# Kernel tuning notes

Hardware: AMD Instinct MI355X
Metric: run time of the kernel (lower is better)

## Reference

```python
import jax, jax.numpy as jnp
import numpy as np

EXTENT = (7, 7)
STRIDE = 1.0
H_IMG, W_IMG, C_IMG = 256, 256, 256
N_BOXES = 1000


def setup_inputs() -> dict:
    key = jax.random.key(0)
    k_img, k_a, k_b = jax.random.split(key, 3)
    image = jax.random.normal(k_img, (1, H_IMG, W_IMG, C_IMG), dtype=jnp.float32)
    # metadata row: (h, w, scale)
    metadata = jnp.array([[float(H_IMG), float(W_IMG), 1.0]], dtype=jnp.float32)
    # valid boxes in pixel coords (x1, y1, x2, y2) with x1<x2, y1<y2
    pa = jax.random.uniform(k_a, (1, N_BOXES, 4), dtype=jnp.float32) * (W_IMG - 1)
    pb = jax.random.uniform(k_b, (1, N_BOXES, 4), dtype=jnp.float32) * (W_IMG - 1)
    lo = jnp.minimum(pa, pb)
    hi = jnp.maximum(pa, pb) + 1.0
    boxes = jnp.stack([lo[..., 0], lo[..., 1],
                       jnp.clip(hi[..., 0], 0, W_IMG - 1),
                       jnp.clip(hi[..., 1], 0, H_IMG - 1)], axis=-1)
    return {"metadata": metadata, "image": image, "boxes": boxes}


def _crop_and_resize(img, nboxes, gh, gw):
    # img: [H, W, C]; nboxes: [N, 4] normalized (y1, x1, y2, x2)
    H, W, C = img.shape
    y1, x1, y2, x2 = nboxes[:, 0], nboxes[:, 1], nboxes[:, 2], nboxes[:, 3]
    ty = jnp.arange(gh, dtype=img.dtype) / (gh - 1)  # [gh]
    tx = jnp.arange(gw, dtype=img.dtype) / (gw - 1)  # [gw]
    in_y = (y1[:, None] + ty[None, :] * (y2 - y1)[:, None]) * (H - 1)  # [N, gh]
    in_x = (x1[:, None] + tx[None, :] * (x2 - x1)[:, None]) * (W - 1)  # [N, gw]
    valid_y = (in_y >= 0) & (in_y <= H - 1)
    valid_x = (in_x >= 0) & (in_x <= W - 1)
    y0f = jnp.floor(in_y)
    x0f = jnp.floor(in_x)
    ly = (in_y - y0f)[:, :, None, None]   # [N, gh, 1, 1]
    lx = (in_x - x0f)[:, None, :, None]   # [N, 1, gw, 1]
    y0 = jnp.clip(y0f, 0, H - 1).astype(jnp.int32)
    y1i = jnp.clip(y0f + 1, 0, H - 1).astype(jnp.int32)
    x0 = jnp.clip(x0f, 0, W - 1).astype(jnp.int32)
    x1i = jnp.clip(x0f + 1, 0, W - 1).astype(jnp.int32)
    yy0, yy1 = y0[:, :, None], y1i[:, :, None]  # [N, gh, 1]
    xx0, xx1 = x0[:, None, :], x1i[:, None, :]  # [N, 1, gw]
    g00 = img[yy0, xx0]  # [N, gh, gw, C]
    g01 = img[yy0, xx1]
    g10 = img[yy1, xx0]
    g11 = img[yy1, xx1]
    top = g00 * (1 - lx) + g01 * lx
    bot = g10 * (1 - lx) + g11 * lx
    out = top * (1 - ly) + bot * ly
    mask = (valid_y[:, :, None] & valid_x[:, None, :])[..., None]
    return jnp.where(mask, out, jnp.zeros((), dtype=img.dtype))


def reference(metadata, image, boxes):
    gh, gw = EXTENT
    b = boxes.astype(jnp.float32) / STRIDE
    h = metadata[0, 0]
    w = metadata[0, 1]
    x1 = b[..., 0] / (w - 1)
    y1 = b[..., 1] / (h - 1)
    x2 = b[..., 2] / (w - 1)
    y2 = b[..., 3] / (h - 1)
    nboxes = jnp.stack([y1, x1, y2, x2], axis=-1).reshape(-1, 4)  # [N, 4]
    slices = _crop_and_resize(image[0], nboxes, gh, gw)  # [N, gh, gw, C]
    return slices[None]  # [1, N, gh, gw, C]
```

## Files before the change

kernel.cpp:

```cpp
#include <hip/hip_runtime.h>

#define GH 7
#define GW 7
#define HIMG 256
#define WIMG 256
#define CIMG 256
#define NBOXES 1000
#define NCELLS (NBOXES * GH * GW)

typedef float f32x4 __attribute__((ext_vector_type(4)));

__global__ __launch_bounds__(256) void roi_kernel(
    const float* __restrict__ meta,
    const float* __restrict__ img,
    const float* __restrict__ boxes,
    float* __restrict__ out)
{
    const int wave = threadIdx.x >> 6;
    const int lane = threadIdx.x & 63;
    const int cell = blockIdx.x * 4 + wave;

    const int b  = cell / (GH * GW);
    const int g  = cell - b * (GH * GW);
    const int gy = g / GW;
    const int gx = g - gy * GW;

    const float h = meta[0];
    const float w = meta[1];

    const float bx1 = boxes[b * 4 + 0] / (w - 1.0f);
    const float by1 = boxes[b * 4 + 1] / (h - 1.0f);
    const float bx2 = boxes[b * 4 + 2] / (w - 1.0f);
    const float by2 = boxes[b * 4 + 3] / (h - 1.0f);

    const float ty = (float)gy / (float)(GH - 1);
    const float tx = (float)gx / (float)(GW - 1);

    const float in_y = (by1 + ty * (by2 - by1)) * (float)(HIMG - 1);
    const float in_x = (bx1 + tx * (bx2 - bx1)) * (float)(WIMG - 1);

    const bool valid = (in_y >= 0.0f) && (in_y <= (float)(HIMG - 1)) &&
                       (in_x >= 0.0f) && (in_x <= (float)(WIMG - 1));

    const float y0f = floorf(in_y);
    const float x0f = floorf(in_x);
    const float ly = in_y - y0f;
    const float lx = in_x - x0f;

    const int y0 = (int)fminf(fmaxf(y0f,        0.0f), (float)(HIMG - 1));
    const int y1 = (int)fminf(fmaxf(y0f + 1.0f, 0.0f), (float)(HIMG - 1));
    const int x0 = (int)fminf(fmaxf(x0f,        0.0f), (float)(WIMG - 1));
    const int x1 = (int)fminf(fmaxf(x0f + 1.0f, 0.0f), (float)(WIMG - 1));

    const f32x4* p00 = (const f32x4*)(img + (size_t)(y0 * WIMG + x0) * CIMG) + lane;
    const f32x4* p01 = (const f32x4*)(img + (size_t)(y0 * WIMG + x1) * CIMG) + lane;
    const f32x4* p10 = (const f32x4*)(img + (size_t)(y1 * WIMG + x0) * CIMG) + lane;
    const f32x4* p11 = (const f32x4*)(img + (size_t)(y1 * WIMG + x1) * CIMG) + lane;

    const f32x4 g00 = *p00;
    const f32x4 g01 = *p01;
    const f32x4 g10 = *p10;
    const f32x4 g11 = *p11;

    const float omlx = 1.0f - lx;
    const float omly = 1.0f - ly;

    f32x4 o = (g00 * omlx + g01 * lx) * omly + (g10 * omlx + g11 * lx) * ly;

    if (!valid) {
        o = (f32x4)0.0f;
    }

    f32x4* op = (f32x4*)(out + (size_t)cell * CIMG) + lane;
    __builtin_nontemporal_store(o, op);
}

extern "C" void kernel_launch(void* const* d_in, const int* in_sizes, int n_in,
                              void* d_out, int out_size, void* d_ws, size_t ws_size,
                              hipStream_t stream) {
    const float* meta  = (const float*)d_in[0];
    const float* img   = (const float*)d_in[1];
    const float* boxes = (const float*)d_in[2];
    float* out = (float*)d_out;

    dim3 grid(NCELLS / 4);
    dim3 block(256);
    roi_kernel<<<grid, block, 0, stream>>>(meta, img, boxes, out);
}
```

Measured before the change: 123.8 us.

## Process two cells per wave and remap blocks for XCD-local box locality

Each wave now handles two adjacent output cells, issuing all eight gather loads before blending, which raises memory-level parallelism per wave and halves the grid size. Block IDs are remapped so that contiguous ranges of logical blocks land on the same XCD (blocks are dispatched round-robin across the 8 XCDs), so neighbouring cells of the same box can share image rows in that XCD's L2. The cost is more registers per thread and a slightly more complex index computation. NBLOCKS divides evenly here, so the mapping covers every cell.

Result: no change. 124.5 us (+0.5%).

```diff
diff --git a/kernel.cpp b/kernel.cpp
--- a/kernel.cpp
+++ b/kernel.cpp
@@ -7,6 +7,9 @@
 #define CIMG 256
 #define NBOXES 1000
 #define NCELLS (NBOXES * GH * GW)
+
+#define CELLS_PER_BLOCK 8
+#define NBLOCKS (NCELLS / CELLS_PER_BLOCK)
 
 typedef float f32x4 __attribute__((ext_vector_type(4)));
 
@@ -18,61 +21,74 @@
 {
     const int wave = threadIdx.x >> 6;
     const int lane = threadIdx.x & 63;
-    const int cell = blockIdx.x * 4 + wave;
 
-    const int b  = cell / (GH * GW);
-    const int g  = cell - b * (GH * GW);
-    const int gy = g / GW;
-    const int gx = g - gy * GW;
+    const int q = NBLOCKS / 8;
+    const int r = NBLOCKS % 8;
+    const int bid = blockIdx.x;
+    const int xcd = bid & 7;
+    const int idx = bid >> 3;
+    const int lb = (xcd < r) ? (xcd * (q + 1) + idx)
+                             : (r * (q + 1) + (xcd - r) * q + idx);
+
+    const int cell0 = lb * CELLS_PER_BLOCK + wave * 2;
 
     const float h = meta[0];
     const float w = meta[1];
 
-    const float bx1 = boxes[b * 4 + 0] / (w - 1.0f);
-    const float by1 = boxes[b * 4 + 1] / (h - 1.0f);
-    const float bx2 = boxes[b * 4 + 2] / (w - 1.0f);
-    const float by2 = boxes[b * 4 + 3] / (h - 1.0f);
+    f32x4 g[2][4];
+    float lxv[2], lyv[2];
+    bool validv[2];
 
-    const float ty = (float)gy / (float)(GH - 1);
-    const float tx = (float)gx / (float)(GW - 1);
+    #pragma unroll
+    for (int c = 0; c < 2; ++c) {
+        const int cell = cell0 + c;
+        const int b  = cell / (GH * GW);
+        const int gg = cell - b * (GH * GW);
+        const int gy = gg / GW;
+        const int gx = gg - gy * GW;
 
-    const float in_y = (by1 + ty * (by2 - by1)) * (float)(HIMG - 1);
-    const float in_x = (bx1 + tx * (bx2 - bx1)) * (float)(WIMG - 1);
+        const float bx1 = boxes[b * 4 + 0] / (w - 1.0f);
+        const float by1 = boxes[b * 4 + 1] / (h - 1.0f);
+        const float bx2 = boxes[b * 4 + 2] / (w - 1.0f);
+        const float by2 = boxes[b * 4 + 3] / (h - 1.0f);
 
-    const bool valid = (in_y >= 0.0f) && (in_y <= (float)(HIMG - 1)) &&
-                       (in_x >= 0.0f) && (in_x <= (float)(WIMG - 1));
+        const float ty = (float)gy / (float)(GH - 1);
+        const float tx = (float)gx / (float)(GW - 1);
 
-    const float y0f = floorf(in_y);
-    const float x0f = floorf(in_x);
-    const float ly = in_y - y0f;
-    const float lx = in_x - x0f;
+        const float in_y = (by1 + ty * (by2 - by1)) * (float)(HIMG - 1);
+        const float in_x = (bx1 + tx * (bx2 - bx1)) * (float)(WIMG - 1);
 
-    const int y0 = (int)fminf(fmaxf(y0f,        0.0f), (float)(HIMG - 1));
-    const int y1 = (int)fminf(fmaxf(y0f + 1.0f, 0.0f), (float)(HIMG - 1));
-    const int x0 = (int)fminf(fmaxf(x0f,        0.0f), (float)(WIMG - 1));
-    const int x1 = (int)fminf(fmaxf(x0f + 1.0f, 0.0f), (float)(WIMG - 1));
+        validv[c] = (in_y >= 0.0f) && (in_y <= (float)(HIMG - 1)) &&
+                    (in_x >= 0.0f) && (in_x <= (float)(WIMG - 1));
 
-    const f32x4* p00 = (const f32x4*)(img + (size_t)(y0 * WIMG + x0) * CIMG) + lane;
-    const f32x4* p01 = (const f32x4*)(img + (size_t)(y0 * WIMG + x1) * CIMG) + lane;
-    const f32x4* p10 = (const f32x4*)(img + (size_t)(y1 * WIMG + x0) * CIMG) + lane;
-    const f32x4* p11 = (const f32x4*)(img + (size_t)(y1 * WIMG + x1) * CIMG) + lane;
+        const float y0f = floorf(in_y);
+        const float x0f = floorf(in_x);
+        lyv[c] = in_y - y0f;
+        lxv[c] = in_x - x0f;
 
-    const f32x4 g00 = *p00;
-    const f32x4 g01 = *p01;
-    const f32x4 g10 = *p10;
-    const f32x4 g11 = *p11;
+        const int y0 = (int)fminf(fmaxf(y0f,        0.0f), (float)(HIMG - 1));
+        const int y1 = (int)fminf(fmaxf(y0f + 1.0f, 0.0f), (float)(HIMG - 1));
+        const int x0 = (int)fminf(fmaxf(x0f,        0.0f), (float)(WIMG - 1));
+        const int x1 = (int)fminf(fmaxf(x0f + 1.0f, 0.0f), (float)(WIMG - 1));
 
-    const float omlx = 1.0f - lx;
-    const float omly = 1.0f - ly;
-
-    f32x4 o = (g00 * omlx + g01 * lx) * omly + (g10 * omlx + g11 * lx) * ly;
-
-    if (!valid) {
-        o = (f32x4)0.0f;
+        g[c][0] = *((const f32x4*)(img + (size_t)(y0 * WIMG + x0) * CIMG) + lane);
+        g[c][1] = *((const f32x4*)(img + (size_t)(y0 * WIMG + x1) * CIMG) + lane);
+        g[c][2] = *((const f32x4*)(img + (size_t)(y1 * WIMG + x0) * CIMG) + lane);
+        g[c][3] = *((const f32x4*)(img + (size_t)(y1 * WIMG + x1) * CIMG) + lane);
     }
 
-    f32x4* op = (f32x4*)(out + (size_t)cell * CIMG) + lane;
-    __builtin_nontemporal_store(o, op);
+    #pragma unroll
+    for (int c = 0; c < 2; ++c) {
+        const float lx = lxv[c], ly = lyv[c];
+        const float omlx = 1.0f - lx, omly = 1.0f - ly;
+
+        f32x4 o = (g[c][0] * omlx + g[c][1] * lx) * omly +
+                  (g[c][2] * omlx + g[c][3] * lx) * ly;
+        if (!validv[c]) o = (f32x4)0.0f;
+
+        f32x4* op = (f32x4*)(out + (size_t)(cell0 + c) * CIMG) + lane;
+        __builtin_nontemporal_store(o, op);
+    }
 }
 
 extern "C" void kernel_launch(void* const* d_in, const int* in_sizes, int n_in,
@@ -83,7 +99,7 @@
     const float* boxes = (const float*)d_in[2];
     float* out = (float*)d_out;
 
-    dim3 grid(NCELLS / 4);
+    dim3 grid(NBLOCKS);
     dim3 block(256);
     roi_kernel<<<grid, block, 0, stream>>>(meta, img, boxes, out);
 }
```
